# Optimization experiments

Hardware: AMD Instinct MI355X
Metric: run time of the kernel (lower is better)

Reference implementation:

```python
import jax, jax.numpy as jnp
import numpy as np

D_MODEL = 512
NUM_HEADS = 8
D_K = D_MODEL // NUM_HEADS


def setup_inputs() -> dict:
    key = jax.random.key(0)
    ks = jax.random.split(key, 10)
    B, L, D = 2, 4096, D_MODEL
    s = 1.0 / np.sqrt(D)
    x = jax.random.normal(ks[0], (B, L, D), dtype=jnp.float32)
    mask = jax.random.randint(ks[1], (B, L), 0, 2, dtype=jnp.int32)
    Wq = jax.random.normal(ks[2], (D, D), dtype=jnp.float32) * s
    bq = jnp.zeros((D,), dtype=jnp.float32)
    Wk = jax.random.normal(ks[3], (D, D), dtype=jnp.float32) * s
    bk = jnp.zeros((D,), dtype=jnp.float32)
    Wv = jax.random.normal(ks[4], (D, D), dtype=jnp.float32) * s
    bv = jnp.zeros((D,), dtype=jnp.float32)
    Wo = jax.random.normal(ks[5], (D, D), dtype=jnp.float32) * s
    bo = jnp.zeros((D,), dtype=jnp.float32)
    return {"x": x, "mask": mask, "Wq": Wq, "bq": bq, "Wk": Wk, "bk": bk,
            "Wv": Wv, "bv": bv, "Wo": Wo, "bo": bo}


def reference(x, mask, Wq, bq, Wk, bk, Wv, bv, Wo, bo):
    B, L, D = x.shape
    H, dk = NUM_HEADS, D_K
    scale = jnp.sqrt(jnp.asarray(dk, dtype=x.dtype))

    def proj(W, b):
        # (B,L,D) @ (D,D) -> (B,H,L,dk)
        return (x @ W.T + b).reshape(B, L, H, dk).transpose(0, 2, 1, 3)

    Q = proj(Wq, bq)
    K = proj(Wk, bk)
    V = proj(Wv, bv)
    scores = jnp.einsum('bhqd,bhkd->bhqk', Q, K) / scale
    # padding mask: (B,L) -> (B,1,1,L); masked positions set to -10000
    m = (mask == 0)[:, None, None, :]
    scores = jnp.where(m, jnp.asarray(-10000.0, dtype=scores.dtype), scores)
    attn = jax.nn.softmax(scores, axis=-1)  # dropout is identity in eval mode
    out = jnp.einsum('bhqk,bhkd->bhqd', attn, V)
    out = out.transpose(0, 2, 1, 3).reshape(B, L, D)
    return out @ Wo.T + bo
```

## Files before the change

### kernel.cpp

```cpp
#include <hip/hip_runtime.h>


#define B_  2
#define L_  4096
#define D_  512
#define H_  8
#define BH_ 16
#define M_  8192

typedef __attribute__((ext_vector_type(8))) short short8;
typedef __attribute__((ext_vector_type(4))) float f32x4;
typedef unsigned short u16;

#if __has_builtin(__builtin_amdgcn_exp2f)
#define EX2(x) __builtin_amdgcn_exp2f(x)
#else
#define EX2(x) exp2f(x)
#endif

static __device__ __forceinline__ u16 f2b(float f) {
    union { float f; unsigned i; } x; x.f = f;
    unsigned r = x.i + 0x7fff + ((x.i >> 16) & 1);
    return (u16)(r >> 16);
}

static __device__ __forceinline__ unsigned cvt_pk_bf16(float lo, float hi) {
    unsigned r;
    asm("v_cvt_pk_bf16_f32 %0, %1, %2" : "=v"(r) : "v"(lo), "v"(hi));
    return r;
}

static __device__ __forceinline__ uint4 pk8(const float4& a, const float4& b) {
    uint4 o;
    o.x = cvt_pk_bf16(a.x, a.y);
    o.y = cvt_pk_bf16(a.z, a.w);
    o.z = cvt_pk_bf16(b.x, b.y);
    o.w = cvt_pk_bf16(b.z, b.w);
    return o;
}

static __device__ __forceinline__ void stage8f(u16* dst, const float* s) {
    const float4 a = *(const float4*)s;
    const float4 b = *(const float4*)(s + 4);
    *(uint4*)dst = pk8(a, b);
}

__global__ __launch_bounds__(256) void kvproj_kernel(
    const float* __restrict__ x,
    const float* __restrict__ Wk, const float* __restrict__ bk,
    const float* __restrict__ Wv, const float* __restrict__ bv,
    u16* __restrict__ Kws, u16* __restrict__ Vws, int bh0)
{
    __shared__ __align__(16) unsigned char sm[10240];
    u16 (*As)[40] = (u16(*)[40])sm;
    u16 (*Bs)[40] = (u16(*)[40])(sm + 5120);
    u16 (*Ts)[73] = (u16(*)[73])sm;

    const int t    = threadIdx.x;
    const int wid  = t >> 6, lane = t & 63;
    const int m15  = lane & 15, quad = lane >> 4;
    const int wm   = wid >> 1, wn = wid & 1;

    const int bh = bh0 + blockIdx.x;
    const int b  = bh >> 3, h = bh & 7;
    const int l0 = blockIdx.y * 64;
    const float* W  = blockIdx.z ? Wv : Wk;
    const float* bi = blockIdx.z ? bv : bk;

    const int lrow = t >> 2;
    const int lcol = (t & 3) * 8;
    const size_t xrow0 = (size_t)b * L_ + l0;

    const float* Ap = x + (xrow0 + lrow) * 512 + lcol;
    const float* Bp = W + (size_t)(h * 64 + lrow) * 512 + lcol;
    float4 a0 = *(const float4*)(Ap), a1 = *(const float4*)(Ap + 4);
    float4 b0 = *(const float4*)(Bp), b1 = *(const float4*)(Bp + 4);

    f32x4 acc[2][2] = {};

    for (int k0 = 0; k0 < 512; k0 += 32) {
        __syncthreads();
        *(uint4*)(&As[lrow][lcol]) = pk8(a0, a1);
        *(uint4*)(&Bs[lrow][lcol]) = pk8(b0, b1);
        __syncthreads();
        if (k0 + 32 < 512) {
            a0 = *(const float4*)(Ap + k0 + 32); a1 = *(const float4*)(Ap + k0 + 36);
            b0 = *(const float4*)(Bp + k0 + 32); b1 = *(const float4*)(Bp + k0 + 36);
        }

        short8 afr[2], bfr[2];
#pragma unroll
        for (int mi = 0; mi < 2; ++mi)
            afr[mi] = *(const short8*)(&As[wm * 32 + mi * 16 + m15][quad * 8]);
#pragma unroll
        for (int ni = 0; ni < 2; ++ni)
            bfr[ni] = *(const short8*)(&Bs[wn * 32 + ni * 16 + m15][quad * 8]);
#pragma unroll
        for (int mi = 0; mi < 2; ++mi)
#pragma unroll
            for (int ni = 0; ni < 2; ++ni)
                acc[mi][ni] = __builtin_amdgcn_mfma_f32_16x16x32_bf16(
                    afr[mi], bfr[ni], acc[mi][ni], 0, 0, 0);
    }

    if (blockIdx.z == 0) {
        u16* out = Kws + (size_t)blockIdx.x * (L_ * 64);
#pragma unroll
        for (int mi = 0; mi < 2; ++mi)
#pragma unroll
            for (int ni = 0; ni < 2; ++ni) {
                const int d  = wn * 32 + ni * 16 + m15;
                const float bv_ = bi[h * 64 + d];
#pragma unroll
                for (int r = 0; r < 4; ++r) {
                    const int l = l0 + wm * 32 + mi * 16 + quad * 4 + r;
                    out[(size_t)l * 64 + d] = f2b(acc[mi][ni][r] + bv_);
                }
            }
    } else {
        __syncthreads();
#pragma unroll
        for (int mi = 0; mi < 2; ++mi)
#pragma unroll
            for (int ni = 0; ni < 2; ++ni) {
                const int d  = wn * 32 + ni * 16 + m15;
                const float bv_ = bi[h * 64 + d];
#pragma unroll
                for (int r = 0; r < 4; ++r)
                    Ts[wm * 32 + mi * 16 + quad * 4 + r][d] = f2b(acc[mi][ni][r] + bv_);
            }
        __syncthreads();
        u16* Vt = Vws + (size_t)blockIdx.x * ((size_t)64 * L_);
        const int d  = t >> 2;
        const int ls = (t & 3) * 16;
        u16 pk[16];
#pragma unroll
        for (int j = 0; j < 16; ++j) pk[j] = Ts[ls + j][d];
        u16* dst = Vt + (size_t)d * L_ + l0 + ls;
        *(uint4*)dst       = *(const uint4*)pk;
        *(uint4*)(dst + 8) = *(const uint4*)(pk + 8);
    }
}

#define KS_OFF  0
#define VTS_OFF 9216
#define PS_OFF  18432
#define PW_PITCH 2368
#define MS_OFF  (PS_OFF + 8 * PW_PITCH)
__global__ __launch_bounds__(512) void attn_kernel(
    const float* __restrict__ x,
    const float* __restrict__ Wq, const float* __restrict__ bq,
    const u16* __restrict__ Kws, const u16* __restrict__ Vws,
    const int* __restrict__ mask,
    float* __restrict__ O, u16* __restrict__ Obf, int bh0)
{
    __shared__ __align__(16) unsigned char sm[MS_OFF + 256];
    u16 (*xs)[40]  = (u16(*)[40])sm;
    u16 (*wqs)[40] = (u16(*)[40])(sm + 10240);
    u16 (*Ks)[72]  = (u16(*)[72])(sm + KS_OFF);
    u16 (*Vts)[72] = (u16(*)[72])(sm + VTS_OFF);
    float* Msb     = (float*)(sm + MS_OFF);

    const int t    = threadIdx.x;
    const int wid  = t >> 6, lane = t & 63;
    const int m15  = lane & 15, quad = lane >> 4;
    u16 (*Psw)[72] = (u16(*)[72])(sm + PS_OFF + wid * PW_PITCH);
    float* Alf     = (float*)(sm + PS_OFF + wid * PW_PITCH + 2304);

    const int bh = bh0 + blockIdx.y;
    const int b  = bh >> 3, h = bh & 7;
    const int q0 = blockIdx.x * 128;
    const u16* Kc  = Kws + (size_t)blockIdx.y * (L_ * 64);
    const u16* Vtc = Vws + (size_t)blockIdx.y * ((size_t)64 * L_);

    f32x4 qacc[4] = {};
    {
        const int xr = t >> 2, xc = (t & 3) * 8;
        const float* xp = x + ((size_t)b * L_ + q0 + xr) * 512 + xc;
        const float* wp = Wq + (size_t)(h * 64 + xr) * 512 + xc;
        float4 xa0 = *(const float4*)xp, xa1 = *(const float4*)(xp + 4);
        float4 wa0 = {}, wa1 = {};
        if (t < 256) { wa0 = *(const float4*)wp; wa1 = *(const float4*)(wp + 4); }
        for (int k0 = 0; k0 < 512; k0 += 32) {
            __syncthreads();
            *(uint4*)(&xs[xr][xc]) = pk8(xa0, xa1);
            if (t < 256) *(uint4*)(&wqs[xr][xc]) = pk8(wa0, wa1);
            __syncthreads();
            if (k0 + 32 < 512) {
                xa0 = *(const float4*)(xp + k0 + 32); xa1 = *(const float4*)(xp + k0 + 36);
                if (t < 256) {
                    wa0 = *(const float4*)(wp + k0 + 32); wa1 = *(const float4*)(wp + k0 + 36);
                }
            }
            const short8 afr = *(const short8*)(&xs[wid * 16 + m15][quad * 8]);
#pragma unroll
            for (int ni = 0; ni < 4; ++ni) {
                const short8 bfr = *(const short8*)(&wqs[ni * 16 + m15][quad * 8]);
                qacc[ni] = __builtin_amdgcn_mfma_f32_16x16x32_bf16(afr, bfr, qacc[ni], 0, 0, 0);
            }
        }
    }
    const float QSCALE = 0.125f * 1.44269504089f;
    short8 qf[2];
#pragma unroll
    for (int ni = 0; ni < 4; ++ni) {
        const float bv_ = bq[h * 64 + ni * 16 + m15];
#pragma unroll
        for (int r = 0; r < 4; ++r)
            Psw[quad * 4 + r][ni * 16 + m15] = f2b((qacc[ni][r] + bv_) * QSCALE);
    }
#pragma unroll
    for (int kc = 0; kc < 2; ++kc)
        qf[kc] = *(const short8*)(&Psw[m15][kc * 32 + quad * 8]);

    const int srow = t >> 3;
    const int scol = (t & 7) * 8;
    uint4 kreg = *(const uint4*)(Kc  + (size_t)srow * 64 + scol);
    uint4 vreg = *(const uint4*)(Vtc + (size_t)srow * L_ + scol);
    int   mreg = (t < 64) ? mask[b * L_ + t] : 0;

    float m_i = -1e30f, l_i = 0.0f;
    f32x4 oacc[4] = {};

    for (int kt = 0; kt < 64; ++kt) {
        __syncthreads();
        *(uint4*)(&Ks [srow][scol]) = kreg;
        *(uint4*)(&Vts[srow][scol]) = vreg;
        if (t < 64) Msb[t] = (mreg == 0) ? -14427.0f : 0.0f;
        __syncthreads();
        if (kt + 1 < 64) {
            const int k1 = (kt + 1) * 64;
            kreg = *(const uint4*)(Kc  + (size_t)(k1 + srow) * 64 + scol);
            vreg = *(const uint4*)(Vtc + (size_t)srow * L_ + k1 + scol);
            if (t < 64) mreg = mask[b * L_ + k1 + t];
        }

        f32x4 s[4];
#pragma unroll
        for (int ni = 0; ni < 4; ++ni) {
            f32x4 sa = *(const f32x4*)(&Msb[ni * 16 + quad * 4]);
#pragma unroll
            for (int kc = 0; kc < 2; ++kc) {
                const short8 kf = *(const short8*)(&Ks[ni * 16 + m15][kc * 32 + quad * 8]);
                sa = __builtin_amdgcn_mfma_f32_16x16x32_bf16(kf, qf[kc], sa, 0, 0, 0);
            }
            s[ni] = sa;
        }

        float mx = fmaxf(
            fmaxf(fmaxf(fmaxf(s[0][0], s[0][1]), fmaxf(s[0][2], s[0][3])),
                  fmaxf(fmaxf(s[1][0], s[1][1]), fmaxf(s[1][2], s[1][3]))),
            fmaxf(fmaxf(fmaxf(s[2][0], s[2][1]), fmaxf(s[2][2], s[2][3])),
                  fmaxf(fmaxf(s[3][0], s[3][1]), fmaxf(s[3][2], s[3][3]))));
        mx = fmaxf(mx, __shfl_xor(mx, 16));
        mx = fmaxf(mx, __shfl_xor(mx, 32));

        if (__any(mx > m_i)) {
            const float mnew = fmaxf(m_i, mx);
            const float a = EX2(m_i - mnew);
            m_i = mnew;
            l_i *= a;
            if (quad == 0) Alf[m15] = a;
            const f32x4 a4 = *(const f32x4*)(&Alf[quad * 4]);
#pragma unroll
            for (int ni = 0; ni < 4; ++ni)
#pragma unroll
                for (int r = 0; r < 4; ++r)
                    oacc[ni][r] *= a4[r];
        }

        float ss = 0.0f;
#pragma unroll
        for (int ni = 0; ni < 4; ++ni) {
            const float p0 = EX2(s[ni][0] - m_i);
            const float p1 = EX2(s[ni][1] - m_i);
            const float p2 = EX2(s[ni][2] - m_i);
            const float p3 = EX2(s[ni][3] - m_i);
            ss += (p0 + p1) + (p2 + p3);
            uint2 w;
            w.x = cvt_pk_bf16(p0, p1);
            w.y = cvt_pk_bf16(p2, p3);
            *(uint2*)(&Psw[m15][ni * 16 + quad * 4]) = w;
        }
        ss += __shfl_xor(ss, 16);
        ss += __shfl_xor(ss, 32);
        l_i += ss;

        short8 pf[2];
#pragma unroll
        for (int kc = 0; kc < 2; ++kc)
            pf[kc] = *(const short8*)(&Psw[m15][kc * 32 + quad * 8]);

#pragma unroll
        for (int ni = 0; ni < 4; ++ni) {
#pragma unroll
            for (int kc = 0; kc < 2; ++kc) {
                const short8 vf = *(const short8*)(&Vts[ni * 16 + m15][kc * 32 + quad * 8]);
                oacc[ni] = __builtin_amdgcn_mfma_f32_16x16x32_bf16(pf[kc], vf, oacc[ni], 0, 0, 0);
            }
        }
    }

    if (quad == 0) Alf[m15] = l_i;
    const f32x4 l4 = *(const f32x4*)(&Alf[quad * 4]);
    if (Obf) {
#pragma unroll
        for (int ni = 0; ni < 4; ++ni)
#pragma unroll
            for (int r = 0; r < 4; ++r) {
                const int qrow = q0 + wid * 16 + quad * 4 + r;
                Obf[((size_t)b * L_ + qrow) * 512 + h * 64 + ni * 16 + m15] =
                    f2b(oacc[ni][r] / l4[r]);
            }
    } else {
#pragma unroll
        for (int ni = 0; ni < 4; ++ni)
#pragma unroll
            for (int r = 0; r < 4; ++r) {
                const int qrow = q0 + wid * 16 + quad * 4 + r;
                O[((size_t)b * L_ + qrow) * 512 + h * 64 + ni * 16 + m15] =
                    oacc[ni][r] / l4[r];
            }
    }
}

__global__ __launch_bounds__(256) void outproj_v2_kernel(
    const u16* __restrict__ AO,
    const float* __restrict__ Wo, const float* __restrict__ bo,
    float* __restrict__ out)
{
    __shared__ __align__(16) u16 As[64][40];
    __shared__ __align__(16) u16 Bs[64][40];

    const int t    = threadIdx.x;
    const int wid  = t >> 6, lane = t & 63;
    const int m15  = lane & 15, quad = lane >> 4;
    const int wm   = wid >> 1, wn = wid & 1;
    const int bm   = blockIdx.x * 64;
    const int n0   = blockIdx.y * 64;

    const int lrow = t >> 2;
    const int lcol = (t & 3) * 8;

    const u16*   Ap = AO + (size_t)(bm + lrow) * 512 + lcol;
    const float* Bp = Wo + (size_t)(n0 + lrow) * 512 + lcol;
    uint4  areg = *(const uint4*)Ap;
    float4 b0 = *(const float4*)Bp, b1 = *(const float4*)(Bp + 4);

    f32x4 acc[2][2] = {};

    for (int k0 = 0; k0 < 512; k0 += 32) {
        __syncthreads();
        *(uint4*)(&As[lrow][lcol]) = areg;
        *(uint4*)(&Bs[lrow][lcol]) = pk8(b0, b1);
        __syncthreads();
        if (k0 + 32 < 512) {
            areg = *(const uint4*)(Ap + k0 + 32);
            b0 = *(const float4*)(Bp + k0 + 32); b1 = *(const float4*)(Bp + k0 + 36);
        }

        short8 afr[2], bfr[2];
#pragma unroll
        for (int mi = 0; mi < 2; ++mi)
            afr[mi] = *(const short8*)(&As[wm * 32 + mi * 16 + m15][quad * 8]);
#pragma unroll
        for (int ni = 0; ni < 2; ++ni)
            bfr[ni] = *(const short8*)(&Bs[wn * 32 + ni * 16 + m15][quad * 8]);
#pragma unroll
        for (int mi = 0; mi < 2; ++mi)
#pragma unroll
            for (int ni = 0; ni < 2; ++ni)
                acc[mi][ni] = __builtin_amdgcn_mfma_f32_16x16x32_bf16(
                    afr[mi], bfr[ni], acc[mi][ni], 0, 0, 0);
    }

#pragma unroll
    for (int mi = 0; mi < 2; ++mi)
#pragma unroll
        for (int ni = 0; ni < 2; ++ni) {
            const int col = n0 + wn * 32 + ni * 16 + m15;
            const float bv_ = bo[col];
#pragma unroll
            for (int r = 0; r < 4; ++r) {
                const int row = bm + wm * 32 + mi * 16 + quad * 4 + r;
                out[(size_t)row * 512 + col] = acc[mi][ni][r] + bv_;
            }
        }
}

__global__ __launch_bounds__(256) void outproj_inplace_kernel(
    float* __restrict__ AO,
    const float* __restrict__ Wo, const float* __restrict__ bo)
{
    __shared__ __align__(16) u16 As[32][520];
    __shared__ __align__(16) u16 Ws_[64][40];

    const int t    = threadIdx.x;
    const int wid  = t >> 6, lane = t & 63;
    const int m15  = lane & 15, quad = lane >> 4;
    const int wm   = wid >> 1, wn = wid & 1;
    const int bm   = blockIdx.x * 32;

#pragma unroll
    for (int it = 0; it < 8; ++it) {
        const int idx = t + it * 256;
        const int row = idx >> 6, c8 = (idx & 63) * 8;
        stage8f(&As[row][c8], AO + (size_t)(bm + row) * 512 + c8);
    }
    const int lrow = t >> 2;
    const int lcol = (t & 3) * 8;
    __syncthreads();

    for (int n0 = 0; n0 < 512; n0 += 64) {
        f32x4 acc[2] = {};
        for (int k0 = 0; k0 < 512; k0 += 32) {
            __syncthreads();
            stage8f(&Ws_[lrow][lcol], Wo + (size_t)(n0 + lrow) * 512 + k0 + lcol);
            __syncthreads();
            const short8 afr = *(const short8*)(&As[wm * 16 + m15][k0 + quad * 8]);
#pragma unroll
            for (int ni = 0; ni < 2; ++ni) {
                const short8 bfr = *(const short8*)(&Ws_[wn * 32 + ni * 16 + m15][quad * 8]);
                acc[ni] = __builtin_amdgcn_mfma_f32_16x16x32_bf16(afr, bfr, acc[ni], 0, 0, 0);
            }
        }
#pragma unroll
        for (int ni = 0; ni < 2; ++ni) {
            const int col = n0 + wn * 32 + ni * 16 + m15;
            const float bv_ = bo[col];
#pragma unroll
            for (int r = 0; r < 4; ++r) {
                const int row = bm + wm * 16 + quad * 4 + r;
                AO[(size_t)row * 512 + col] = acc[ni][r] + bv_;
            }
        }
    }
}

extern "C" void kernel_launch(void* const* d_in, const int* in_sizes, int n_in,
                              void* d_out, int out_size, void* d_ws, size_t ws_size,
                              hipStream_t stream) {
    const float* x    = (const float*)d_in[0];
    const int*   mask = (const int*)d_in[1];
    const float* Wq = (const float*)d_in[2]; const float* bq = (const float*)d_in[3];
    const float* Wk = (const float*)d_in[4]; const float* bk = (const float*)d_in[5];
    const float* Wv = (const float*)d_in[6]; const float* bv = (const float*)d_in[7];
    const float* Wo = (const float*)d_in[8]; const float* bo = (const float*)d_in[9];

    float* out = (float*)d_out;
    u16*   ws  = (u16*)d_ws;

    const size_t per_bh   = (size_t)2 * L_ * 64 * 2;
    const size_t kv_bytes = (size_t)BH_ * per_bh;
    const size_t ao_bytes = (size_t)M_ * 512 * 2;

    if (ws_size >= kv_bytes + ao_bytes) {
        u16* Kws  = ws;
        u16* Vws  = Kws + (size_t)BH_ * (L_ * 64);
        u16* AOws = ws + kv_bytes / 2;
        kvproj_kernel<<<dim3(BH_, L_ / 64, 2), 256, 0, stream>>>(
            x, Wk, bk, Wv, bv, Kws, Vws, 0);
        attn_kernel<<<dim3(L_ / 128, BH_), 512, 0, stream>>>(
            x, Wq, bq, Kws, Vws, mask, out, AOws, 0);
        outproj_v2_kernel<<<dim3(M_ / 64, 8), 256, 0, stream>>>(AOws, Wo, bo, out);
    } else {
        int chunk = 16;
        while (chunk > 1 && (size_t)chunk * per_bh > ws_size) chunk >>= 1;
        u16* Kws = ws;
        u16* Vws = Kws + (size_t)chunk * (L_ * 64);
        for (int bh0 = 0; bh0 < BH_; bh0 += chunk) {
            kvproj_kernel<<<dim3(chunk, L_ / 64, 2), 256, 0, stream>>>(
                x, Wk, bk, Wv, bv, Kws, Vws, bh0);
            attn_kernel<<<dim3(L_ / 128, chunk), 512, 0, stream>>>(
                x, Wq, bq, Kws, Vws, mask, out, nullptr, bh0);
        }
        outproj_inplace_kernel<<<dim3(M_ / 32), 256, 0, stream>>>(out, Wo, bo);
    }
}
```

Before: 271.5 us.

## Rework attention inner loop with 32x32 MFMA and split-KV across waves

The attention kernel moves from 16x16x32 to 32x32x16 bf16 MFMA. Each wave now handles 32 queries against half of each 64-key tile, and the two KV halves are merged at the end through shared memory. The P fragments for the PV product are built in registers with cross-lane shuffles instead of a round trip through shared memory. K/V tiles use an XOR-swizzled unpadded layout to avoid bank conflicts, and launch bounds request 4 blocks per CU. This cuts LDS traffic and raises MFMA efficiency, at the cost of a final merge step and more register pressure.

```diff
diff --git a/kernel.cpp b/kernel.cpp
--- a/kernel.cpp
+++ b/kernel.cpp
@@ -8,8 +8,9 @@
 #define BH_ 16
 #define M_  8192
 
-typedef __attribute__((ext_vector_type(8))) short short8;
-typedef __attribute__((ext_vector_type(4))) float f32x4;
+typedef __attribute__((ext_vector_type(8)))  short short8;
+typedef __attribute__((ext_vector_type(4)))  float f32x4;
+typedef __attribute__((ext_vector_type(16))) float f32x16;
 typedef unsigned short u16;
 
 #if __has_builtin(__builtin_amdgcn_exp2f)
@@ -43,6 +44,13 @@
     const float4 a = *(const float4*)s;
     const float4 b = *(const float4*)(s + 4);
     *(uint4*)dst = pk8(a, b);
+}
+
+static __device__ __forceinline__ short8 mk8(unsigned a, unsigned b,
+                                             unsigned c, unsigned d) {
+    union { unsigned u[4]; short8 s; } x;
+    x.u[0] = a; x.u[1] = b; x.u[2] = c; x.u[3] = d;
+    return x.s;
 }
 
 __global__ __launch_bounds__(256) void kvproj_kernel(
@@ -142,36 +150,44 @@
     }
 }
 
-#define KS_OFF  0
-#define VTS_OFF 9216
-#define PS_OFF  18432
-#define PW_PITCH 2368
-#define MS_OFF  (PS_OFF + 8 * PW_PITCH)
-__global__ __launch_bounds__(512) void attn_kernel(
+__global__ __launch_bounds__(512, 4) void attn_kernel(
     const float* __restrict__ x,
     const float* __restrict__ Wq, const float* __restrict__ bq,
     const u16* __restrict__ Kws, const u16* __restrict__ Vws,
     const int* __restrict__ mask,
     float* __restrict__ O, u16* __restrict__ Obf, int bh0)
 {
-    __shared__ __align__(16) unsigned char sm[MS_OFF + 256];
+    __shared__ __align__(16) unsigned char sm[34816];
     u16 (*xs)[40]  = (u16(*)[40])sm;
     u16 (*wqs)[40] = (u16(*)[40])(sm + 10240);
-    u16 (*Ks)[72]  = (u16(*)[72])(sm + KS_OFF);
-    u16 (*Vts)[72] = (u16(*)[72])(sm + VTS_OFF);
-    float* Msb     = (float*)(sm + MS_OFF);
+    u16 (*Qs)[72]  = (u16(*)[72])sm;
+    u16 (*Ks)[64]  = (u16(*)[64])sm;
+    u16 (*Vts)[64] = (u16(*)[64])(sm + 8192);
+    float* Msb     = (float*)(sm + 16384);
 
     const int t    = threadIdx.x;
     const int wid  = t >> 6, lane = t & 63;
     const int m15  = lane & 15, quad = lane >> 4;
-    u16 (*Psw)[72] = (u16(*)[72])(sm + PS_OFF + wid * PW_PITCH);
-    float* Alf     = (float*)(sm + PS_OFF + wid * PW_PITCH + 2304);
+    const int l5   = lane & 31, hi = lane >> 5;
+    const int hi4  = hi * 4;
+    const int x7   = l5 & 7;
+    const int qg   = wid & 3;
+    const int kb   = wid >> 2;
+    float* AlfR    = (float*)(sm + 16640) + wid * 32;
 
     const int bh = bh0 + blockIdx.y;
     const int b  = bh >> 3, h = bh & 7;
     const int q0 = blockIdx.x * 128;
     const u16* Kc  = Kws + (size_t)blockIdx.y * (L_ * 64);
     const u16* Vtc = Vws + (size_t)blockIdx.y * ((size_t)64 * L_);
+
+    const int srow  = t >> 3;
+    const int scol8 = (t & 7);
+    const int sslot = (scol8 ^ (srow & 7)) * 8;
+
+    uint4 kreg = *(const uint4*)(Kc + (size_t)srow * 64 + scol8 * 8);
+    uint4 vreg = *(const uint4*)(Vtc + (size_t)srow * L_ + scol8 * 8);
+    int   mreg = (t < 64) ? mask[b * L_ + t] : 0;
 
     f32x4 qacc[4] = {};
     {
@@ -200,59 +216,62 @@
             }
         }
     }
+
     const float QSCALE = 0.125f * 1.44269504089f;
-    short8 qf[2];
+    __syncthreads();
 #pragma unroll
     for (int ni = 0; ni < 4; ++ni) {
         const float bv_ = bq[h * 64 + ni * 16 + m15];
 #pragma unroll
         for (int r = 0; r < 4; ++r)
-            Psw[quad * 4 + r][ni * 16 + m15] = f2b((qacc[ni][r] + bv_) * QSCALE);
-    }
-#pragma unroll
-    for (int kc = 0; kc < 2; ++kc)
-        qf[kc] = *(const short8*)(&Psw[m15][kc * 32 + quad * 8]);
-
-    const int srow = t >> 3;
-    const int scol = (t & 7) * 8;
-    uint4 kreg = *(const uint4*)(Kc  + (size_t)srow * 64 + scol);
-    uint4 vreg = *(const uint4*)(Vtc + (size_t)srow * L_ + scol);
-    int   mreg = (t < 64) ? mask[b * L_ + t] : 0;
+            Qs[wid * 16 + quad * 4 + r][ni * 16 + m15] =
+                f2b((qacc[ni][r] + bv_) * QSCALE);
+    }
+    __syncthreads();
+    short8 qfr[4];
+#pragma unroll
+    for (int kd = 0; kd < 4; ++kd)
+        qfr[kd] = *(const short8*)(&Qs[32 * qg + l5][16 * kd + 8 * hi]);
+    __syncthreads();
 
     float m_i = -1e30f, l_i = 0.0f;
-    f32x4 oacc[4] = {};
+    f32x16 oacc[2];
+#pragma unroll
+    for (int db = 0; db < 2; ++db)
+#pragma unroll
+        for (int e = 0; e < 16; ++e) oacc[db][e] = 0.0f;
 
     for (int kt = 0; kt < 64; ++kt) {
         __syncthreads();
-        *(uint4*)(&Ks [srow][scol]) = kreg;
-        *(uint4*)(&Vts[srow][scol]) = vreg;
+        *(uint4*)(&Ks [srow][sslot]) = kreg;
+        *(uint4*)(&Vts[srow][sslot]) = vreg;
         if (t < 64) Msb[t] = (mreg == 0) ? -14427.0f : 0.0f;
         __syncthreads();
         if (kt + 1 < 64) {
             const int k1 = (kt + 1) * 64;
-            kreg = *(const uint4*)(Kc  + (size_t)(k1 + srow) * 64 + scol);
-            vreg = *(const uint4*)(Vtc + (size_t)srow * L_ + k1 + scol);
+            kreg = *(const uint4*)(Kc + (size_t)(k1 + srow) * 64 + scol8 * 8);
+            vreg = *(const uint4*)(Vtc + (size_t)srow * L_ + k1 + scol8 * 8);
             if (t < 64) mreg = mask[b * L_ + k1 + t];
         }
 
-        f32x4 s[4];
-#pragma unroll
-        for (int ni = 0; ni < 4; ++ni) {
-            f32x4 sa = *(const f32x4*)(&Msb[ni * 16 + quad * 4]);
-#pragma unroll
-            for (int kc = 0; kc < 2; ++kc) {
-                const short8 kf = *(const short8*)(&Ks[ni * 16 + m15][kc * 32 + quad * 8]);
-                sa = __builtin_amdgcn_mfma_f32_16x16x32_bf16(kf, qf[kc], sa, 0, 0, 0);
-            }
-            s[ni] = sa;
+        f32x16 sa;
+#pragma unroll
+        for (int p = 0; p < 4; ++p) {
+            const f32x4 bb = *(const f32x4*)(&Msb[32 * kb + 8 * p + hi4]);
+            sa[4*p+0] = bb[0]; sa[4*p+1] = bb[1]; sa[4*p+2] = bb[2]; sa[4*p+3] = bb[3];
+        }
+#pragma unroll
+        for (int kd = 0; kd < 4; ++kd) {
+            const short8 kf = *(const short8*)(
+                &Ks[32 * kb + l5][(((2 * kd + hi) ^ x7)) * 8]);
+            sa = __builtin_amdgcn_mfma_f32_32x32x16_bf16(kf, qfr[kd], sa, 0, 0, 0);
         }
 
         float mx = fmaxf(
-            fmaxf(fmaxf(fmaxf(s[0][0], s[0][1]), fmaxf(s[0][2], s[0][3])),
-                  fmaxf(fmaxf(s[1][0], s[1][1]), fmaxf(s[1][2], s[1][3]))),
-            fmaxf(fmaxf(fmaxf(s[2][0], s[2][1]), fmaxf(s[2][2], s[2][3])),
-                  fmaxf(fmaxf(s[3][0], s[3][1]), fmaxf(s[3][2], s[3][3]))));
-        mx = fmaxf(mx, __shfl_xor(mx, 16));
+            fmaxf(fmaxf(fmaxf(sa[0], sa[1]),  fmaxf(sa[2], sa[3])),
+                  fmaxf(fmaxf(sa[4], sa[5]),  fmaxf(sa[6], sa[7]))),
+            fmaxf(fmaxf(fmaxf(sa[8], sa[9]),  fmaxf(sa[10], sa[11])),
+                  fmaxf(fmaxf(sa[12], sa[13]), fmaxf(sa[14], sa[15]))));
         mx = fmaxf(mx, __shfl_xor(mx, 32));
 
         if (__any(mx > m_i)) {
@@ -260,67 +279,102 @@
             const float a = EX2(m_i - mnew);
             m_i = mnew;
             l_i *= a;
-            if (quad == 0) Alf[m15] = a;
-            const f32x4 a4 = *(const f32x4*)(&Alf[quad * 4]);
-#pragma unroll
-            for (int ni = 0; ni < 4; ++ni)
-#pragma unroll
-                for (int r = 0; r < 4; ++r)
-                    oacc[ni][r] *= a4[r];
-        }
-
-        float ss = 0.0f;
-#pragma unroll
-        for (int ni = 0; ni < 4; ++ni) {
-            const float p0 = EX2(s[ni][0] - m_i);
-            const float p1 = EX2(s[ni][1] - m_i);
-            const float p2 = EX2(s[ni][2] - m_i);
-            const float p3 = EX2(s[ni][3] - m_i);
-            ss += (p0 + p1) + (p2 + p3);
-            uint2 w;
-            w.x = cvt_pk_bf16(p0, p1);
-            w.y = cvt_pk_bf16(p2, p3);
-            *(uint2*)(&Psw[m15][ni * 16 + quad * 4]) = w;
-        }
-        ss += __shfl_xor(ss, 16);
+            if (hi == 0) AlfR[l5] = a;
+#pragma unroll
+            for (int p = 0; p < 4; ++p) {
+                const f32x4 a4 = *(const f32x4*)(&AlfR[8 * p + hi4]);
+#pragma unroll
+                for (int i = 0; i < 4; ++i) {
+                    oacc[0][4*p+i] *= a4[i];
+                    oacc[1][4*p+i] *= a4[i];
+                }
+            }
+        }
+
+        float pv[16];
+#pragma unroll
+        for (int r = 0; r < 16; ++r) pv[r] = EX2(sa[r] - m_i);
+        float ss = ((pv[0]+pv[1]) + (pv[2]+pv[3])) + ((pv[4]+pv[5]) + (pv[6]+pv[7]))
+                 + ((pv[8]+pv[9]) + (pv[10]+pv[11])) + ((pv[12]+pv[13]) + (pv[14]+pv[15]));
         ss += __shfl_xor(ss, 32);
         l_i += ss;
 
-        short8 pf[2];
-#pragma unroll
-        for (int kc = 0; kc < 2; ++kc)
-            pf[kc] = *(const short8*)(&Psw[m15][kc * 32 + quad * 8]);
-
-#pragma unroll
-        for (int ni = 0; ni < 4; ++ni) {
-#pragma unroll
-            for (int kc = 0; kc < 2; ++kc) {
-                const short8 vf = *(const short8*)(&Vts[ni * 16 + m15][kc * 32 + quad * 8]);
-                oacc[ni] = __builtin_amdgcn_mfma_f32_16x16x32_bf16(pf[kc], vf, oacc[ni], 0, 0, 0);
-            }
-        }
-    }
-
-    if (quad == 0) Alf[m15] = l_i;
-    const f32x4 l4 = *(const f32x4*)(&Alf[quad * 4]);
-    if (Obf) {
-#pragma unroll
-        for (int ni = 0; ni < 4; ++ni)
-#pragma unroll
-            for (int r = 0; r < 4; ++r) {
-                const int qrow = q0 + wid * 16 + quad * 4 + r;
-                Obf[((size_t)b * L_ + qrow) * 512 + h * 64 + ni * 16 + m15] =
-                    f2b(oacc[ni][r] / l4[r]);
-            }
-    } else {
-#pragma unroll
-        for (int ni = 0; ni < 4; ++ni)
-#pragma unroll
-            for (int r = 0; r < 4; ++r) {
-                const int qrow = q0 + wid * 16 + quad * 4 + r;
-                O[((size_t)b * L_ + qrow) * 512 + h * 64 + ni * 16 + m15] =
-                    oacc[ni][r] / l4[r];
-            }
+        unsigned W[8];
+#pragma unroll
+        for (int m = 0; m < 8; ++m) W[m] = cvt_pk_bf16(pv[2*m], pv[2*m+1]);
+
+#pragma unroll
+        for (int c1 = 0; c1 < 2; ++c1) {
+            const unsigned X  = hi ? W[4*c1+0] : W[4*c1+2];
+            const unsigned Y  = hi ? W[4*c1+1] : W[4*c1+3];
+            const unsigned Xp = __shfl_xor((int)X, 32);
+            const unsigned Yp = __shfl_xor((int)Y, 32);
+            const unsigned w0 = hi ? Xp : W[4*c1+0];
+            const unsigned w1 = hi ? Yp : W[4*c1+1];
+            const unsigned w2 = hi ? W[4*c1+2] : Xp;
+            const unsigned w3 = hi ? W[4*c1+3] : Yp;
+            const short8 af = mk8(w0, w1, w2, w3);
+            const int kcg = 2 * kb + c1;
+#pragma unroll
+            for (int db = 0; db < 2; ++db) {
+                const short8 vf = *(const short8*)(
+                    &Vts[32 * db + l5][(((2 * kcg + hi) ^ x7)) * 8]);
+                oacc[db] = __builtin_amdgcn_mfma_f32_32x32x16_bf16(af, vf, oacc[db], 0, 0, 0);
+            }
+        }
+    }
+
+    float* Op  = (float*)sm;
+    float* Mp0 = (float*)(sm + 32768);
+    float* Mp1 = Mp0 + 128;
+    float* FA  = (float*)(sm + 33792);
+    float* FB  = FA + 128;
+
+    __syncthreads();
+    if (wid >= 4) {
+#pragma unroll
+        for (int db = 0; db < 2; ++db) {
+            const int d = 32 * db + l5;
+#pragma unroll
+            for (int p = 0; p < 4; ++p) {
+                const int qb   = 32 * qg + 8 * p + hi4;
+                const int slot = (qb >> 2) ^ l5;
+                f32x4 v;
+#pragma unroll
+                for (int i = 0; i < 4; ++i) v[i] = oacc[db][4*p+i];
+                *(f32x4*)(&Op[d * 128 + slot * 4]) = v;
+            }
+        }
+        if (hi == 0) { Mp0[32 * qg + l5] = m_i; Mp1[32 * qg + l5] = l_i; }
+    }
+    __syncthreads();
+    if (wid < 4) {
+        const int q5 = 32 * qg + l5;
+        const float mB = Mp0[q5], lB = Mp1[q5];
+        const float mS = fmaxf(m_i, mB);
+        const float aA = EX2(m_i - mS), aB = EX2(mB - mS);
+        const float linv = 1.0f / (l_i * aA + lB * aB);
+        if (hi == 0) { FA[q5] = aA * linv; FB[q5] = aB * linv; }
+#pragma unroll
+        for (int db = 0; db < 2; ++db) {
+            const int d = 32 * db + l5;
+            const int col = h * 64 + d;
+#pragma unroll
+            for (int p = 0; p < 4; ++p) {
+                const int qb   = 32 * qg + 8 * p + hi4;
+                const f32x4 fa = *(const f32x4*)(&FA[qb]);
+                const f32x4 fb = *(const f32x4*)(&FB[qb]);
+                const int slot = (qb >> 2) ^ l5;
+                const f32x4 ob = *(const f32x4*)(&Op[d * 128 + slot * 4]);
+#pragma unroll
+                for (int i = 0; i < 4; ++i) {
+                    const float val = oacc[db][4*p+i] * fa[i] + ob[i] * fb[i];
+                    const size_t row = (size_t)b * L_ + q0 + qb + i;
+                    if (Obf) Obf[row * 512 + col] = f2b(val);
+                    else     O  [row * 512 + col] = val;
+                }
+            }
+        }
     }
 }
 
```

New measurement: 250.5 us. 1.08x faster.
